# Kernel tuning notes

Measured on AMD Instinct MI355X. Metric: run time of the kernel, lower is better.

## Reference

```python
import jax, jax.numpy as jnp
import numpy as np

B, S, E, D = 2, 1024, 1024, 2048
H, KV, HD = 8, 4, 256
SOFTCAP = 50.0
SCALE = 256.0 ** -0.5  # query_pre_attn_scalar ** -0.5
WINDOW = 512
EPS = 1e-6
THETA = 10000.0


def setup_inputs() -> dict:
    key = jax.random.key(0)
    ks = jax.random.split(key, 10)
    hidden_states = jax.random.normal(ks[0], (B, S, D), jnp.float32)
    encoder_hidden_states = jax.random.normal(ks[1], (B, E, D), jnp.float32)
    # two packed segments per sequence (position resets at S//2)
    position_ids = jnp.broadcast_to(
        jnp.concatenate([jnp.arange(S // 2), jnp.arange(S - S // 2)]), (B, S)
    ).astype(jnp.int32)
    decoder_attention_mask = jnp.ones((B, S), jnp.int32)
    encoder_attention_mask = jnp.broadcast_to(
        (jnp.arange(E) < (E - 64)).astype(jnp.int32), (B, E))
    # RoPE tables from position ids
    inv_freq = 1.0 / (THETA ** (jnp.arange(0, HD, 2, dtype=jnp.float32) / HD))
    freqs = position_ids.astype(jnp.float32)[..., None] * inv_freq  # [B,S,HD/2]
    emb = jnp.concatenate([freqs, freqs], axis=-1)  # [B,S,HD]
    cos, sin = jnp.cos(emb), jnp.sin(emb)
    wq = 0.02 * jax.random.normal(ks[2], (D, H * HD), jnp.float32)
    wk = 0.02 * jax.random.normal(ks[3], (D, KV * HD), jnp.float32)
    wv = 0.02 * jax.random.normal(ks[4], (D, KV * HD), jnp.float32)
    wo = 0.02 * jax.random.normal(ks[5], (H * HD, D), jnp.float32)
    q_norm_w = 0.1 * jax.random.normal(ks[6], (HD,), jnp.float32)
    k_norm_w = 0.1 * jax.random.normal(ks[7], (HD,), jnp.float32)
    return dict(hidden_states=hidden_states,
                encoder_hidden_states=encoder_hidden_states,
                cos=cos, sin=sin, wq=wq, wk=wk, wv=wv, wo=wo,
                q_norm_w=q_norm_w, k_norm_w=k_norm_w,
                decoder_attention_mask=decoder_attention_mask,
                encoder_attention_mask=encoder_attention_mask,
                position_ids=position_ids)


def _rms_norm(x, w):
    # GemmaRMSNorm: x * rsqrt(mean(x^2)+eps) * (1 + w)
    var = jnp.mean(x * x, axis=-1, keepdims=True)
    return x * jax.lax.rsqrt(var + EPS) * (1.0 + w)


def _rotate_half(x):
    h = x.shape[-1] // 2
    return jnp.concatenate([-x[..., h:], x[..., :h]], axis=-1)


def _build_merged_mask(dec_mask, enc_mask, position_ids):
    dm = dec_mask.astype(bool)
    em = enc_mask.astype(bool)
    Sq = dm.shape[1]
    causal = jnp.tril(jnp.ones((Sq, Sq), bool))
    # segment ids from non-increasing position resets (packing)
    reset = jnp.concatenate(
        [jnp.ones((dm.shape[0], 1), bool),
         position_ids[:, 1:] <= position_ids[:, :-1]], axis=1)
    seg = jnp.cumsum(reset.astype(jnp.int32), axis=1)
    block = seg[:, :, None] == seg[:, None, :]
    full_self = dm[:, None, :] & causal[None] & block  # [B,S,S]
    rows = jnp.arange(Sq)
    dist = rows[:, None] - rows[None, :]
    sliding = (dist >= 0) & (dist < WINDOW)
    self_mask = full_self & sliding[None]
    cross = jnp.broadcast_to(em[:, None, :], (dm.shape[0], Sq, em.shape[1]))
    return jnp.concatenate([self_mask, cross], axis=-1)[:, None]  # [B,1,S,S+E]


def reference(hidden_states, encoder_hidden_states, cos, sin, wq, wk, wv, wo,
              q_norm_w, k_norm_w, decoder_attention_mask,
              encoder_attention_mask, position_ids):
    Bq, Sq, _ = hidden_states.shape
    Ek = encoder_hidden_states.shape[1]
    q = (hidden_states @ wq).reshape(Bq, Sq, H, HD).transpose(0, 2, 1, 3)
    k_self = (hidden_states @ wk).reshape(Bq, Sq, KV, HD).transpose(0, 2, 1, 3)
    v_self = (hidden_states @ wv).reshape(Bq, Sq, KV, HD).transpose(0, 2, 1, 3)
    k_cross = (encoder_hidden_states @ wk).reshape(Bq, Ek, KV, HD).transpose(0, 2, 1, 3)
    v_cross = (encoder_hidden_states @ wv).reshape(Bq, Ek, KV, HD).transpose(0, 2, 1, 3)
    # QK RMSNorm (cross keys normalized but NOT rotated, matching source)
    q = _rms_norm(q, q_norm_w)
    k_self = _rms_norm(k_self, k_norm_w)
    k_cross = _rms_norm(k_cross, k_norm_w)
    c, s = cos[:, None, :, :], sin[:, None, :, :]
    q = q * c + _rotate_half(q) * s
    k_self = k_self * c + _rotate_half(k_self) * s
    k = jnp.concatenate([k_self, k_cross], axis=2)  # [B,KV,S+E,HD]
    v = jnp.concatenate([v_self, v_cross], axis=2)
    rep = H // KV
    k = jnp.repeat(k, rep, axis=1)
    v = jnp.repeat(v, rep, axis=1)
    mask = _build_merged_mask(decoder_attention_mask, encoder_attention_mask,
                              position_ids)
    scores = jnp.einsum('bhqd,bhkd->bhqk', q, k) * SCALE
    scores = SOFTCAP * jnp.tanh(scores / SOFTCAP)  # logit softcapping
    scores = jnp.where(mask, scores, jnp.float32(-1e30))
    attn = jax.nn.softmax(scores, axis=-1)
    out = jnp.einsum('bhqk,bhkd->bhqd', attn, v)
    out = out.transpose(0, 2, 1, 3).reshape(Bq, Sq, H * HD)
    return out @ wo
```

## Files before the change

### kernel.cpp

```cpp
#include <hip/hip_runtime.h>
#include <math.h>

#define B_ 2
#define S_ 1024
#define E_ 1024
#define D_ 2048
#define H_ 8
#define KV_ 4
#define HD_ 256
#define WINDOW_ 512u
#define SCALE_ 0.0625f
#define CAP_ 50.0f
#define EPS_ 1e-6f
#define CROSS_OK (-7)
#define KINV (-2147483647 - 1)

typedef __bf16 bf8_t __attribute__((ext_vector_type(8)));
typedef float fx4 __attribute__((ext_vector_type(4)));
#define MFMA16(a, b, c) __builtin_amdgcn_mfma_f32_16x16x32_bf16((a), (b), (c), 0, 0, 0)

typedef __attribute__((address_space(1))) unsigned int gas_u32;
typedef __attribute__((address_space(3))) unsigned int las_u32;
__device__ __forceinline__ void gl2lds16(const void* g, void* l) {
    __builtin_amdgcn_global_load_lds((const gas_u32*)g, (las_u32*)l, 16, 0, 0);
}

union U4 { __bf16 b[4]; unsigned long long u; };

__device__ __forceinline__ float pexp(float dot) {
    float e = __expf(dot * (2.0f * SCALE_ / CAP_));
    return __expf(-(2.0f * CAP_) / (e + 1.0f));
}

__global__ __launch_bounds__(256) void tobf16(const float* __restrict__ x,
                                              __bf16* __restrict__ y, int n4) {
    int i = blockIdx.x * 256 + threadIdx.x;
    if (i >= n4) return;
    float4 v = ((const float4*)x)[i];
    U4 p;
    p.b[0] = (__bf16)v.x; p.b[1] = (__bf16)v.y;
    p.b[2] = (__bf16)v.z; p.b[3] = (__bf16)v.w;
    *(unsigned long long*)&y[(size_t)i * 4] = p.u;
}

__global__ __launch_bounds__(256) void tsplit(const float* __restrict__ W,
                                              __bf16* __restrict__ Th,
                                              __bf16* __restrict__ Tl, int K, int N) {
    __shared__ float tile[32][33];
    const int t = threadIdx.x, tx = t & 31, ty = t >> 5;
    const int k0 = blockIdx.x * 32, n0 = blockIdx.y * 32;
#pragma unroll
    for (int r = 0; r < 4; ++r)
        tile[ty + r * 8][tx] = W[(size_t)(k0 + ty + r * 8) * N + n0 + tx];
    __syncthreads();
#pragma unroll
    for (int r = 0; r < 4; ++r) {
        float v = tile[tx][ty + r * 8];
        __bf16 h = (__bf16)v;
        size_t o = (size_t)(n0 + ty + r * 8) * K + k0 + tx;
        Th[o] = h;
        Tl[o] = (__bf16)(v - (float)h);
    }
}

template <int NPASS>
__device__ __forceinline__ void gemm_core2(
    const __bf16* __restrict__ Ah, const __bf16* __restrict__ Al,
    const __bf16* __restrict__ Bh, const __bf16* __restrict__ Bl,
    int row0, int col0, int K,
    __bf16* As0, __bf16* As1, __bf16* Bs0, __bf16* Bs1, fx4 (&acc)[4][4]) {
    const int tid = threadIdx.x, lane = tid & 63, wv = tid >> 6;
    const int l15 = lane & 15, lq = lane >> 4;
    const int wm = (wv >> 1) * 64, wn = (wv & 1) * 64;
    constexpr int WCNT = (NPASS == 1) ? 0x0F74 : (NPASS == 2) ? 0x0F76 : 0x0F78;

    auto stage = [&](int buf, int k0) {
#pragma unroll
        for (int s = 0; s < 2; ++s) {
            int ch = (wv * 2 + s) * 64 + lane;
            int r = ch >> 2, cp = ch & 3;
            int cl = (cp - ((r >> 1) & 3)) & 3;
            size_t ga = (size_t)(row0 + r) * K + k0 + cl * 8;
            size_t gb = (size_t)(col0 + r) * K + k0 + cl * 8;
            gl2lds16(Ah + ga, As0 + buf * 4096 + ch * 8);
            if (NPASS >= 3) gl2lds16(Al + ga, As1 + buf * 4096 + ch * 8);
            gl2lds16(Bh + gb, Bs0 + buf * 4096 + ch * 8);
            if (NPASS >= 2) gl2lds16(Bl + gb, Bs1 + buf * 4096 + ch * 8);
        }
    };

    stage(0, 0);
    for (int k0 = 0; k0 < K; k0 += 32) {
        const int buf = (k0 >> 5) & 1;
        const bool hasnext = (k0 + 32 < K);
        if (hasnext) stage(buf ^ 1, k0 + 32);
        if (hasnext) __builtin_amdgcn_s_waitcnt(WCNT);
        else         __builtin_amdgcn_s_waitcnt(0x0F70);
        __builtin_amdgcn_s_barrier();
        __builtin_amdgcn_sched_barrier(0);

        const __bf16* A0 = As0 + buf * 4096;
        const __bf16* A1 = As1 + buf * 4096;
        const __bf16* B0 = Bs0 + buf * 4096;
        const __bf16* B1 = Bs1 + buf * 4096;
        bf8_t ah[4], al[4], bh[4], bl[4];
#pragma unroll
        for (int i = 0; i < 4; ++i) {
            int row = wm + i * 16 + l15;
            int sl = row * 4 + ((lq + (row >> 1)) & 3);
            ah[i] = *(const bf8_t*)(A0 + sl * 8);
            if (NPASS >= 3) al[i] = *(const bf8_t*)(A1 + sl * 8);
        }
#pragma unroll
        for (int j = 0; j < 4; ++j) {
            int row = wn + j * 16 + l15;
            int sl = row * 4 + ((lq + (row >> 1)) & 3);
            bh[j] = *(const bf8_t*)(B0 + sl * 8);
            if (NPASS >= 2) bl[j] = *(const bf8_t*)(B1 + sl * 8);
        }
#pragma unroll
        for (int i = 0; i < 4; ++i)
#pragma unroll
            for (int j = 0; j < 4; ++j) {
                acc[i][j] = MFMA16(ah[i], bh[j], acc[i][j]);
                if (NPASS >= 2) acc[i][j] = MFMA16(ah[i], bl[j], acc[i][j]);
                if (NPASS >= 3) acc[i][j] = MFMA16(al[i], bh[j], acc[i][j]);
            }
        __builtin_amdgcn_sched_barrier(0);
        __builtin_amdgcn_s_barrier();
    }
}

__global__ __launch_bounds__(256) void gemm_proj(
    const __bf16* __restrict__ hsb, const __bf16* __restrict__ encb,
    const __bf16* __restrict__ BTh, const __bf16* __restrict__ BTl,
    float* __restrict__ qf32, float* __restrict__ ksf, float* __restrict__ kcf,
    __bf16* __restrict__ vtS, __bf16* __restrict__ vtC) {
    __shared__ __bf16 As0[8192], Bs0[8192], Bs1[8192];
    const int bx = blockIdx.x, row0 = blockIdx.y * 128;
    const __bf16* A;
    float* Ck; __bf16* Cv; int col0;
    if (bx < 32) { A = hsb;  col0 = bx * 128;               Ck = ksf; Cv = vtS; }
    else         { A = encb; col0 = (bx - 32) * 128 + 2048; Ck = kcf; Cv = vtC; }
    fx4 acc[4][4];
#pragma unroll
    for (int i = 0; i < 4; ++i)
#pragma unroll
        for (int j = 0; j < 4; ++j) acc[i][j] = (fx4){0.f, 0.f, 0.f, 0.f};
    if (col0 >= 3072)
        gemm_core2<2>(A, nullptr, BTh, BTl, row0, col0, D_, As0, nullptr, Bs0, Bs1, acc);
    else
        gemm_core2<1>(A, nullptr, BTh, BTl, row0, col0, D_, As0, nullptr, Bs0, Bs1, acc);

    const int tid = threadIdx.x, lane = tid & 63, wv = tid >> 6;
    const int l15 = lane & 15, lq = lane >> 4;
    const int wm = (wv >> 1) * 64, wn = (wv & 1) * 64;
    const int mode = (col0 < 2048) ? 0 : (col0 < 3072 ? 1 : 2);
#pragma unroll
    for (int i = 0; i < 4; ++i)
#pragma unroll
        for (int j = 0; j < 4; ++j) {
            int mb = row0 + wm + i * 16 + lq * 4;
            int n = col0 + wn + j * 16 + l15;
            if (mode == 0) {
#pragma unroll
                for (int r = 0; r < 4; ++r)
                    qf32[(size_t)(mb + r) * 2048 + n] = acc[i][j][r];
            } else if (mode == 1) {
                int nk = n - 2048;
#pragma unroll
                for (int r = 0; r < 4; ++r)
                    Ck[(size_t)(mb + r) * 1024 + nk] = acc[i][j][r];
            } else {
                int nv = n - 3072;
                int b = mb >> 10, s = mb & 1023;
                int kv = nv >> 8, d = nv & 255;
                U4 pk;
#pragma unroll
                for (int r = 0; r < 4; ++r) pk.b[r] = (__bf16)acc[i][j][r];
                *(unsigned long long*)&Cv[((size_t)(b * KV_ + kv) * HD_ + d) * 1024 + s] = pk.u;
            }
        }
}

__global__ __launch_bounds__(256) void gemm_out(
    const __bf16* __restrict__ Ah, const __bf16* __restrict__ Al,
    const __bf16* __restrict__ Bh, const __bf16* __restrict__ Bl,
    float* __restrict__ C) {
    __shared__ __bf16 As0[8192], As1[8192], Bs0[8192], Bs1[8192];
    const int row0 = blockIdx.y * 128, col0 = blockIdx.x * 128;
    fx4 acc[4][4];
#pragma unroll
    for (int i = 0; i < 4; ++i)
#pragma unroll
        for (int j = 0; j < 4; ++j) acc[i][j] = (fx4){0.f, 0.f, 0.f, 0.f};
    gemm_core2<3>(Ah, Al, Bh, Bl, row0, col0, 2048, As0, As1, Bs0, Bs1, acc);
    const int tid = threadIdx.x, lane = tid & 63, wv = tid >> 6;
    const int l15 = lane & 15, lq = lane >> 4;
    const int wm = (wv >> 1) * 64, wn = (wv & 1) * 64;
#pragma unroll
    for (int i = 0; i < 4; ++i)
#pragma unroll
        for (int j = 0; j < 4; ++j) {
            int mb = row0 + wm + i * 16 + lq * 4;
            int n = col0 + wn + j * 16 + l15;
#pragma unroll
            for (int r = 0; r < 4; ++r)
                C[(size_t)(mb + r) * 2048 + n] = acc[i][j][r];
        }
}

__global__ __launch_bounds__(256) void rmsnorm_rope(const float* __restrict__ x,
                                                    __bf16* __restrict__ out,
                                                    const float* __restrict__ w,
                                                    const float* __restrict__ cs,
                                                    const float* __restrict__ sn,
                                                    int nheads, int do_rope, int trans) {
    const int tid = threadIdx.x;
    const size_t base = (size_t)blockIdx.x * HD_;
    float v = x[base + tid];
    float ss = v * v;
#pragma unroll
    for (int off = 32; off; off >>= 1) ss += __shfl_down(ss, off);
    __shared__ float red[4];
    __shared__ float ybuf[HD_];
    const int lane = tid & 63, wvi = tid >> 6;
    if (lane == 0) red[wvi] = ss;
    __syncthreads();
    float tot = red[0] + red[1] + red[2] + red[3];
    float scale = rsqrtf(tot * (1.0f / HD_) + EPS_);
    float y = v * scale * (1.0f + w[tid]);
    const int m = blockIdx.x / nheads;
    if (do_rope) {
        ybuf[tid] = y;
        __syncthreads();
        float rot = (tid < HD_ / 2) ? -ybuf[tid + HD_ / 2] : ybuf[tid - HD_ / 2];
        size_t coff = (size_t)m * HD_;
        y = y * cs[coff + tid] + rot * sn[coff + tid];
    }
    size_t oidx;
    if (trans) {
        int hh = blockIdx.x % nheads;
        int b = m >> 10, s = m & 1023;
        oidx = ((size_t)(b * nheads + hh) * 1024 + s) * HD_ + tid;
    } else {
        oidx = base + tid;
    }
    out[oidx] = (__bf16)y;
}

__global__ void segscan(const int* __restrict__ pos, const int* __restrict__ dm,
                        const int* __restrict__ em, int* __restrict__ seg,
                        int* __restrict__ ki) {
    const int b = blockIdx.x, s = threadIdx.x;
    __shared__ int sh[1024];
    int p = pos[b * S_ + s];
    int r = (s == 0) ? 1 : (p <= pos[b * S_ + s - 1] ? 1 : 0);
    sh[s] = r;
    __syncthreads();
    for (int off = 1; off < 1024; off <<= 1) {
        int v = sh[s];
        int u = (s >= off) ? sh[s - off] : 0;
        __syncthreads();
        sh[s] = v + u;
        __syncthreads();
    }
    int sv = sh[s];
    seg[b * S_ + s] = sv;
    ki[b * 2048 + s] = dm[b * S_ + s] ? sv : KINV;
    ki[b * 2048 + 1024 + s] = em[b * E_ + s] ? CROSS_OK : KINV;
}

__global__ __launch_bounds__(256, 1) void attn_part(
    const __bf16* __restrict__ qb,
    const __bf16* __restrict__ kb,
    const __bf16* __restrict__ kcb,
    const __bf16* __restrict__ vtS,
    const __bf16* __restrict__ vtC,
    const int* __restrict__ seg, const int* __restrict__ ki,
    float* __restrict__ accS, float* __restrict__ accC,
    float* __restrict__ lsS, float* __restrict__ lsC) {
    __shared__ __bf16 Ks[2][8192];
    __shared__ __bf16 Vs[2][8192];
    __shared__ __bf16 Ps[4][640];
    __shared__ int kinfoS[1024];
    const int tid = threadIdx.x, lane = tid & 63, wv = tid >> 6;
    const int l15 = lane & 15, lq = lane >> 4;
    const int bid = blockIdx.x;
    const int role = bid >> 8;
    const int g = bid & 7;
    const int b = g >> 2, kv = g & 3;
    const int rest = (bid >> 3) & 31;
    const int qt = rest >> 1, h = kv * 2 + (rest & 1);
    const int s0 = qt * 64;

    int lo = 0, nt = 32;
    const __bf16 *Kbase, *Vbase;
    if (role == 0) {
        lo = (s0 >= 512) ? ((s0 - 511) & ~31) : 0;
        nt = (s0 + 64 - lo) >> 5;
        Kbase = kb + (size_t)(b * KV_ + kv) * (1024 * 256);
        Vbase = vtS + (size_t)(b * KV_ + kv) * (256 * 1024);
    } else {
        Kbase = kcb + (size_t)(b * KV_ + kv) * (1024 * 256);
        Vbase = vtC + (size_t)(b * KV_ + kv) * (256 * 1024);
    }
    const int nk = nt * 32;
    const int kiofs = b * 2048 + (role ? 1024 : lo);
    for (int i = tid; i < nk; i += 256) kinfoS[i] = ki[kiofs + i];
    __syncthreads();

    const int qpos = s0 + wv * 16 + l15;
    bf8_t qf[8];
    const __bf16* qrow = qb + ((size_t)(b * S_ + qpos) * H_ + h) * HD_;
#pragma unroll
    for (int f = 0; f < 8; ++f) qf[f] = *(const bf8_t*)(qrow + f * 32 + lq * 8);
    const int tgt = role ? CROSS_OK : seg[b * S_ + qpos];

    auto stage = [&](int buf, int t) {
        const __bf16* Kt = Kbase + (size_t)(lo + t * 32) * 256;
        const __bf16* Vt = Vbase + (lo + t * 32);
#pragma unroll
        for (int r = 0; r < 4; ++r) {
            int cid = r * 256 + tid;
            int key = cid >> 5, c = cid & 31;
            gl2lds16(Kt + key * 256 + (((c ^ (key & 7))) << 3), &Ks[buf][cid * 8]);
        }
#pragma unroll
        for (int r = 0; r < 4; ++r) {
            int cid = r * 256 + tid;
            int d = cid >> 2, kc = cid & 3;
            gl2lds16(Vt + (size_t)d * 1024 + ((kc ^ ((d >> 1) & 3)) << 3),
                     &Vs[buf][cid * 8]);
        }
    };

    fx4 accO[16];
#pragma unroll
    for (int j = 0; j < 16; ++j) accO[j] = (fx4){0.f, 0.f, 0.f, 0.f};
    float lsum = 0.f;
    const int swzk = l15 & 7;
    const int swzv = lq ^ ((l15 >> 1) & 3);

    stage(0, 0);
    for (int i = 0; i < nt; ++i) {
        const int kt0_c = lo + i * 32;
        const int kio_c = i * 32;
        const bool hasnext = (i + 1 < nt);
        if (hasnext) stage((i + 1) & 1, i + 1);
        if (hasnext) __builtin_amdgcn_s_waitcnt(0x0F78);
        else         __builtin_amdgcn_s_waitcnt(0x0F70);
        __builtin_amdgcn_s_barrier();
        __builtin_amdgcn_sched_barrier(0);

        const __bf16* Ksb = Ks[i & 1];
        const __bf16* Vsb = Vs[i & 1];
        fx4 sc0 = (fx4){0.f, 0.f, 0.f, 0.f}, sc1 = (fx4){0.f, 0.f, 0.f, 0.f};
#pragma unroll
        for (int f = 0; f < 8; ++f) {
            bf8_t k0 = *(const bf8_t*)&Ksb[(l15 * 32 + ((f * 4 + lq) ^ swzk)) * 8];
            bf8_t k1 = *(const bf8_t*)&Ksb[((16 + l15) * 32 + ((f * 4 + lq) ^ swzk)) * 8];
            sc0 = MFMA16(k0, qf[f], sc0);
            sc1 = MFMA16(k1, qf[f], sc1);
        }
        int4 ki0 = *(const int4*)&kinfoS[kio_c + lq * 4];
        int4 ki1 = *(const int4*)&kinfoS[kio_c + 16 + lq * 4];
        int ka0[4] = {ki0.x, ki0.y, ki0.z, ki0.w};
        int ka1[4] = {ki1.x, ki1.y, ki1.z, ki1.w};
        U4 p0, p1;
#pragma unroll
        for (int r = 0; r < 4; ++r) {
            int key0 = kt0_c + lq * 4 + r;
            float e0 = pexp(sc0[r]);
            float e1 = pexp(sc1[r]);
            bool ok0 = (ka0[r] == tgt) && (role || (unsigned)(qpos - key0) < WINDOW_);
            bool ok1 = (ka1[r] == tgt) && (role || (unsigned)(qpos - key0 - 16) < WINDOW_);
            float v0 = ok0 ? e0 : 0.f;
            float v1 = ok1 ? e1 : 0.f;
            lsum += v0 + v1;
            p0.b[r] = (__bf16)v0;
            p1.b[r] = (__bf16)v1;
        }
        *(unsigned long long*)&Ps[wv][l15 * 40 + lq * 4] = p0.u;
        *(unsigned long long*)&Ps[wv][l15 * 40 + 16 + lq * 4] = p1.u;
        bf8_t pf = *(const bf8_t*)&Ps[wv][l15 * 40 + lq * 8];
#pragma unroll
        for (int j = 0; j < 16; ++j) {
            bf8_t vb = *(const bf8_t*)&Vsb[((j * 16 + l15) * 4 + swzv) * 8];
            accO[j] = MFMA16(pf, vb, accO[j]);
        }
        __builtin_amdgcn_sched_barrier(0);
        __builtin_amdgcn_s_barrier();
    }

    lsum += __shfl_xor(lsum, 16, 64);
    lsum += __shfl_xor(lsum, 32, 64);
    float* accT = role ? accC : accS;
    float* lsT  = role ? lsC  : lsS;
    if (lq == 0) lsT[(size_t)(b * S_ + qpos) * 8 + h] = lsum;
#pragma unroll
    for (int j = 0; j < 16; ++j)
#pragma unroll
        for (int r = 0; r < 4; ++r) {
            size_t idx = (size_t)(b * S_ + s0 + wv * 16 + lq * 4 + r) * 2048 +
                         h * 256 + j * 16 + l15;
            accT[idx] = accO[j][r];
        }
}

__global__ __launch_bounds__(256) void combine(
    const float* __restrict__ aS, const float* __restrict__ aC,
    const float* __restrict__ lS, const float* __restrict__ lC,
    __bf16* __restrict__ aH, __bf16* __restrict__ aL) {
    int i = blockIdx.x * 256 + threadIdx.x;
    size_t base = (size_t)i * 4;
    int row = (int)(base >> 11);
    int h = (int)((base >> 8) & 7);
    float inv = 1.0f / (lS[row * 8 + h] + lC[row * 8 + h]);
    float4 a = ((const float4*)aS)[i];
    float4 c = ((const float4*)aC)[i];
    float o[4] = {(a.x + c.x) * inv, (a.y + c.y) * inv,
                  (a.z + c.z) * inv, (a.w + c.w) * inv};
    U4 ph, pl;
#pragma unroll
    for (int r = 0; r < 4; ++r) {
        __bf16 hi = (__bf16)o[r];
        ph.b[r] = hi;
        pl.b[r] = (__bf16)(o[r] - (float)hi);
    }
    *(unsigned long long*)&aH[base] = ph.u;
    *(unsigned long long*)&aL[base] = pl.u;
}

extern "C" void kernel_launch(void* const* d_in, const int* in_sizes, int n_in,
                              void* d_out, int out_size, void* d_ws, size_t ws_size,
                              hipStream_t stream) {
    (void)in_sizes; (void)n_in; (void)out_size; (void)ws_size;
    const float* hs  = (const float*)d_in[0];
    const float* enc = (const float*)d_in[1];
    const float* cs  = (const float*)d_in[2];
    const float* sn  = (const float*)d_in[3];
    const float* wq  = (const float*)d_in[4];
    const float* wk  = (const float*)d_in[5];
    const float* wv  = (const float*)d_in[6];
    const float* wo  = (const float*)d_in[7];
    const float* qnw = (const float*)d_in[8];
    const float* knw = (const float*)d_in[9];
    const int* dm    = (const int*)d_in[10];
    const int* em    = (const int*)d_in[11];
    const int* pos   = (const int*)d_in[12];
    float* out = (float*)d_out;

    char* ws = (char*)d_ws;
    const size_t MB = 1ull << 20;
    __bf16* hs_bf   = (__bf16*)(ws + 0 * MB);
    __bf16* enc_bf  = (__bf16*)(ws + 8 * MB);
    __bf16* wqkvTH  = (__bf16*)(ws + 16 * MB);
    __bf16* wqkvTL  = (__bf16*)(ws + 32 * MB);
    __bf16* woTH    = (__bf16*)(ws + 48 * MB);
    __bf16* woTL    = (__bf16*)(ws + 56 * MB);
    float*  qf32    = (float*)(ws + 64 * MB);
    float*  ksf     = (float*)(ws + 80 * MB);
    float*  kcf     = (float*)(ws + 88 * MB);
    __bf16* k_bf    = (__bf16*)(ws + 104 * MB);
    __bf16* kc_bf   = (__bf16*)(ws + 108 * MB);
    __bf16* vtS     = (__bf16*)(ws + 112 * MB);
    __bf16* vtC     = (__bf16*)(ws + 116 * MB);
    int*    seg     = (int*)(ws + 120 * MB);
    int*    kinfo   = (int*)(ws + 121 * MB);
    __bf16* q_bf    = (__bf16*)(ws + 124 * MB);
    __bf16* aoutH   = (__bf16*)(ws + 0 * MB);
    __bf16* aoutL   = (__bf16*)(ws + 9 * MB);
    float*  accS    = (float*)(ws + 64 * MB);
    float*  accC    = (float*)(ws + 81 * MB);
    float*  lsS     = (float*)(ws + 98 * MB);
    float*  lsC     = (float*)(ws + 99 * MB);

    const int M = B_ * S_;

    tobf16<<<4096, 256, 0, stream>>>(hs, hs_bf, M * D_ / 4);
    tobf16<<<4096, 256, 0, stream>>>(enc, enc_bf, M * D_ / 4);
    tsplit<<<dim3(64, 64), 256, 0, stream>>>(wq, wqkvTH, wqkvTL, D_, 2048);
    tsplit<<<dim3(64, 32), 256, 0, stream>>>(wk, wqkvTH + (size_t)2048 * 2048,
                                             wqkvTL + (size_t)2048 * 2048, D_, 1024);
    tsplit<<<dim3(64, 32), 256, 0, stream>>>(wv, wqkvTH + (size_t)3072 * 2048,
                                             wqkvTL + (size_t)3072 * 2048, D_, 1024);
    tsplit<<<dim3(64, 64), 256, 0, stream>>>(wo, woTH, woTL, 2048, D_);

    gemm_proj<<<dim3(48, 16), 256, 0, stream>>>(hs_bf, enc_bf, wqkvTH, wqkvTL,
                                                qf32, ksf, kcf, vtS, vtC);

    rmsnorm_rope<<<16384, 256, 0, stream>>>(qf32, q_bf, qnw, cs, sn, H_, 1, 0);
    rmsnorm_rope<<<8192, 256, 0, stream>>>(ksf, k_bf, knw, cs, sn, KV_, 1, 1);
    rmsnorm_rope<<<8192, 256, 0, stream>>>(kcf, kc_bf, knw, cs, sn, KV_, 0, 1);
    segscan<<<B_, 1024, 0, stream>>>(pos, dm, em, seg, kinfo);

    attn_part<<<512, 256, 0, stream>>>(q_bf, k_bf, kc_bf, vtS, vtC, seg, kinfo,
                                       accS, accC, lsS, lsC);
    combine<<<4096, 256, 0, stream>>>(accS, accC, lsS, lsC, aoutH, aoutL);

    gemm_out<<<dim3(16, 16), 256, 0, stream>>>(aoutH, aoutL, woTH, woTL, out);
}
```

Measured before the change: 428.6 us.

## Merge prep launches, skip unused weight low halves, enlarge projection GEMM tiles

Folds the two bf16 conversions, four weight transpose-splits and the segment scan into a single prep kernel. The low-half bf16 writes for wq and wk are dropped, since the projection GEMM only does the high pass for those columns. The segment scan is rewritten with wave shuffles instead of a 1024-thread shared-memory scan. The QKV projection GEMM moves to 512-thread blocks covering 256 rows, reusing each B tile across more rows, and the three RMSNorm/RoPE launches become one. The aim is to cut launch overhead and memory traffic, at the cost of more branching in the merged kernels and fewer, larger GEMM blocks.

```diff
diff --git a/kernel.cpp b/kernel.cpp
--- a/kernel.cpp
+++ b/kernel.cpp
@@ -32,9 +32,8 @@
     return __expf(-(2.0f * CAP_) / (e + 1.0f));
 }
 
-__global__ __launch_bounds__(256) void tobf16(const float* __restrict__ x,
-                                              __bf16* __restrict__ y, int n4) {
-    int i = blockIdx.x * 256 + threadIdx.x;
+__device__ __forceinline__ void dev_tobf16(const float* __restrict__ x,
+                                           __bf16* __restrict__ y, int n4, int i) {
     if (i >= n4) return;
     float4 v = ((const float4*)x)[i];
     U4 p;
@@ -43,12 +42,13 @@
     *(unsigned long long*)&y[(size_t)i * 4] = p.u;
 }
 
-__global__ __launch_bounds__(256) void tsplit(const float* __restrict__ W,
-                                              __bf16* __restrict__ Th,
-                                              __bf16* __restrict__ Tl, int K, int N) {
-    __shared__ float tile[32][33];
-    const int t = threadIdx.x, tx = t & 31, ty = t >> 5;
-    const int k0 = blockIdx.x * 32, n0 = blockIdx.y * 32;
+__device__ __forceinline__ void dev_tsplit(const float* __restrict__ W,
+                                           __bf16* __restrict__ Th,
+                                           __bf16* __restrict__ Tl, int K, int N,
+                                           int bx, int by, int t,
+                                           float (*tile)[33], int wlo) {
+    const int tx = t & 31, ty = t >> 5;
+    const int k0 = bx * 32, n0 = by * 32;
 #pragma unroll
     for (int r = 0; r < 4; ++r)
         tile[ty + r * 8][tx] = W[(size_t)(k0 + ty + r * 8) * N + n0 + tx];
@@ -59,8 +59,89 @@
         __bf16 h = (__bf16)v;
         size_t o = (size_t)(n0 + ty + r * 8) * K + k0 + tx;
         Th[o] = h;
-        Tl[o] = (__bf16)(v - (float)h);
-    }
+        if (wlo) Tl[o] = (__bf16)(v - (float)h);
+    }
+}
+
+__device__ __forceinline__ void dev_segscan(const int* __restrict__ pos,
+                                            const int* __restrict__ dm,
+                                            const int* __restrict__ em,
+                                            int* __restrict__ seg,
+                                            int* __restrict__ ki,
+                                            int b, int t, int* wsum) {
+    const int base = b * 1024 + t * 4;
+    int4 p = *(const int4*)&pos[base];
+    int pm1 = (t == 0) ? 0 : pos[base - 1];
+    int r0 = (t == 0) ? 1 : (p.x <= pm1 ? 1 : 0);
+    int r1 = (p.y <= p.x), r2 = (p.z <= p.y), r3 = (p.w <= p.z);
+    int c0 = r0, c1 = c0 + r1, c2 = c1 + r2, c3 = c2 + r3;
+    const int lane = t & 63, wv = t >> 6;
+    int x = c3;
+#pragma unroll
+    for (int off = 1; off < 64; off <<= 1) {
+        int y = __shfl_up(x, off, 64);
+        if (lane >= off) x += y;
+    }
+    if (lane == 63) wsum[wv] = x;
+    __syncthreads();
+    int woff = 0;
+#pragma unroll
+    for (int w = 0; w < 4; ++w) if (w < wv) woff += wsum[w];
+    const int excl = woff + x - c3;
+    int sv[4] = {excl + c0, excl + c1, excl + c2, excl + c3};
+    int4 dmv = *(const int4*)&dm[base];
+    int4 emv = *(const int4*)&em[base];
+    int dma[4] = {dmv.x, dmv.y, dmv.z, dmv.w};
+    int ema[4] = {emv.x, emv.y, emv.z, emv.w};
+#pragma unroll
+    for (int r = 0; r < 4; ++r) {
+        seg[base + r] = sv[r];
+        ki[b * 2048 + t * 4 + r] = dma[r] ? sv[r] : KINV;
+        ki[b * 2048 + 1024 + t * 4 + r] = ema[r] ? CROSS_OK : KINV;
+    }
+}
+
+__global__ __launch_bounds__(256) void prep(
+    const float* __restrict__ hs, const float* __restrict__ enc,
+    const float* __restrict__ wq, const float* __restrict__ wk,
+    const float* __restrict__ wvp, const float* __restrict__ wo,
+    const int* __restrict__ pos, const int* __restrict__ dm,
+    const int* __restrict__ em,
+    __bf16* __restrict__ hs_bf, __bf16* __restrict__ enc_bf,
+    __bf16* __restrict__ wqkvTH, __bf16* __restrict__ wqkvTL,
+    __bf16* __restrict__ woTH, __bf16* __restrict__ woTL,
+    int* __restrict__ seg, int* __restrict__ ki) {
+    __shared__ float tile[32][33];
+    __shared__ int wsum[4];
+    int bid = blockIdx.x;
+    const int t = threadIdx.x;
+    if (bid < 4096) { dev_tobf16(hs, hs_bf, 1048576, bid * 256 + t); return; }
+    bid -= 4096;
+    if (bid < 4096) { dev_tobf16(enc, enc_bf, 1048576, bid * 256 + t); return; }
+    bid -= 4096;
+    if (bid < 4096) {
+        dev_tsplit(wq, wqkvTH, nullptr, 2048, 2048, bid & 63, bid >> 6, t, tile, 0);
+        return;
+    }
+    bid -= 4096;
+    if (bid < 2048) {
+        dev_tsplit(wk, wqkvTH + (size_t)2048 * 2048, nullptr, 2048, 1024,
+                   bid & 63, bid >> 6, t, tile, 0);
+        return;
+    }
+    bid -= 2048;
+    if (bid < 2048) {
+        dev_tsplit(wvp, wqkvTH + (size_t)3072 * 2048, wqkvTL + (size_t)3072 * 2048,
+                   2048, 1024, bid & 63, bid >> 6, t, tile, 1);
+        return;
+    }
+    bid -= 2048;
+    if (bid < 4096) {
+        dev_tsplit(wo, woTH, woTL, 2048, 2048, bid & 63, bid >> 6, t, tile, 1);
+        return;
+    }
+    bid -= 4096;
+    dev_segscan(pos, dm, em, seg, ki, bid, t, wsum);
 }
 
 template <int NPASS>
@@ -131,13 +212,82 @@
     }
 }
 
-__global__ __launch_bounds__(256) void gemm_proj(
+template <int NPASS>
+__device__ __forceinline__ void gemm_core3(
+    const __bf16* __restrict__ Ah,
+    const __bf16* __restrict__ Bh, const __bf16* __restrict__ Bl,
+    int row0, int col0, int K,
+    __bf16* As0, __bf16* Bs0, __bf16* Bs1, fx4 (&acc)[4][4]) {
+    const int tid = threadIdx.x, lane = tid & 63, wv = tid >> 6;
+    const int l15 = lane & 15, lq = lane >> 4;
+    const int wm = (wv >> 1) * 64, wn = (wv & 1) * 64;
+    constexpr int WCNT = (NPASS == 1) ? 0x0F73 : 0x0F74;
+
+    auto stage = [&](int buf, int k0) {
+#pragma unroll
+        for (int s = 0; s < 2; ++s) {
+            int ch = s * 512 + tid;
+            int r = ch >> 2, cp = ch & 3;
+            int cl = (cp - ((r >> 1) & 3)) & 3;
+            size_t ga = (size_t)(row0 + r) * K + k0 + cl * 8;
+            gl2lds16(Ah + ga, As0 + buf * 8192 + ch * 8);
+        }
+        {
+            int ch = tid;
+            int r = ch >> 2, cp = ch & 3;
+            int cl = (cp - ((r >> 1) & 3)) & 3;
+            size_t gb = (size_t)(col0 + r) * K + k0 + cl * 8;
+            gl2lds16(Bh + gb, Bs0 + buf * 4096 + ch * 8);
+            if (NPASS >= 2) gl2lds16(Bl + gb, Bs1 + buf * 4096 + ch * 8);
+        }
+    };
+
+    stage(0, 0);
+    for (int k0 = 0; k0 < K; k0 += 32) {
+        const int buf = (k0 >> 5) & 1;
+        const bool hasnext = (k0 + 32 < K);
+        if (hasnext) stage(buf ^ 1, k0 + 32);
+        if (hasnext) __builtin_amdgcn_s_waitcnt(WCNT);
+        else         __builtin_amdgcn_s_waitcnt(0x0F70);
+        __builtin_amdgcn_s_barrier();
+        __builtin_amdgcn_sched_barrier(0);
+
+        const __bf16* A0 = As0 + buf * 8192;
+        const __bf16* B0 = Bs0 + buf * 4096;
+        const __bf16* B1 = Bs1 + buf * 4096;
+        bf8_t ah[4], bh[4], bl[4];
+#pragma unroll
+        for (int i = 0; i < 4; ++i) {
+            int row = wm + i * 16 + l15;
+            int sl = row * 4 + ((lq + (row >> 1)) & 3);
+            ah[i] = *(const bf8_t*)(A0 + sl * 8);
+        }
+#pragma unroll
+        for (int j = 0; j < 4; ++j) {
+            int row = wn + j * 16 + l15;
+            int sl = row * 4 + ((lq + (row >> 1)) & 3);
+            bh[j] = *(const bf8_t*)(B0 + sl * 8);
+            if (NPASS >= 2) bl[j] = *(const bf8_t*)(B1 + sl * 8);
+        }
+#pragma unroll
+        for (int i = 0; i < 4; ++i)
+#pragma unroll
+            for (int j = 0; j < 4; ++j) {
+                acc[i][j] = MFMA16(ah[i], bh[j], acc[i][j]);
+                if (NPASS >= 2) acc[i][j] = MFMA16(ah[i], bl[j], acc[i][j]);
+            }
+        __builtin_amdgcn_sched_barrier(0);
+        __builtin_amdgcn_s_barrier();
+    }
+}
+
+__global__ __launch_bounds__(512) void gemm_proj(
     const __bf16* __restrict__ hsb, const __bf16* __restrict__ encb,
     const __bf16* __restrict__ BTh, const __bf16* __restrict__ BTl,
     float* __restrict__ qf32, float* __restrict__ ksf, float* __restrict__ kcf,
     __bf16* __restrict__ vtS, __bf16* __restrict__ vtC) {
-    __shared__ __bf16 As0[8192], Bs0[8192], Bs1[8192];
-    const int bx = blockIdx.x, row0 = blockIdx.y * 128;
+    __shared__ __bf16 As0[16384], Bs0[8192], Bs1[8192];
+    const int bx = blockIdx.x, row0 = blockIdx.y * 256;
     const __bf16* A;
     float* Ck; __bf16* Cv; int col0;
     if (bx < 32) { A = hsb;  col0 = bx * 128;               Ck = ksf; Cv = vtS; }
@@ -148,9 +298,9 @@
 #pragma unroll
         for (int j = 0; j < 4; ++j) acc[i][j] = (fx4){0.f, 0.f, 0.f, 0.f};
     if (col0 >= 3072)
-        gemm_core2<2>(A, nullptr, BTh, BTl, row0, col0, D_, As0, nullptr, Bs0, Bs1, acc);
+        gemm_core3<2>(A, BTh, BTl, row0, col0, D_, As0, Bs0, Bs1, acc);
     else
-        gemm_core2<1>(A, nullptr, BTh, BTl, row0, col0, D_, As0, nullptr, Bs0, Bs1, acc);
+        gemm_core3<1>(A, BTh, BTl, row0, col0, D_, As0, Bs0, Bs1, acc);
 
     const int tid = threadIdx.x, lane = tid & 63, wv = tid >> 6;
     const int l15 = lane & 15, lq = lane >> 4;
@@ -210,14 +360,21 @@
         }
 }
 
-__global__ __launch_bounds__(256) void rmsnorm_rope(const float* __restrict__ x,
-                                                    __bf16* __restrict__ out,
-                                                    const float* __restrict__ w,
-                                                    const float* __restrict__ cs,
-                                                    const float* __restrict__ sn,
-                                                    int nheads, int do_rope, int trans) {
+__global__ __launch_bounds__(256) void rms_all(
+    const float* __restrict__ qf32, const float* __restrict__ ksf,
+    const float* __restrict__ kcf,
+    __bf16* __restrict__ q_bf, __bf16* __restrict__ k_bf,
+    __bf16* __restrict__ kc_bf,
+    const float* __restrict__ qnw, const float* __restrict__ knw,
+    const float* __restrict__ cs, const float* __restrict__ sn) {
+    int bid = blockIdx.x;
+    const float* x; __bf16* out; const float* w;
+    int nheads, do_rope, trans;
+    if (bid < 16384)      { x = qf32; out = q_bf;  w = qnw; nheads = 8; do_rope = 1; trans = 0; }
+    else if (bid < 24576) { bid -= 16384; x = ksf; out = k_bf;  w = knw; nheads = 4; do_rope = 1; trans = 1; }
+    else                  { bid -= 24576; x = kcf; out = kc_bf; w = knw; nheads = 4; do_rope = 0; trans = 1; }
     const int tid = threadIdx.x;
-    const size_t base = (size_t)blockIdx.x * HD_;
+    const size_t base = (size_t)bid * HD_;
     float v = x[base + tid];
     float ss = v * v;
 #pragma unroll
@@ -230,7 +387,7 @@
     float tot = red[0] + red[1] + red[2] + red[3];
     float scale = rsqrtf(tot * (1.0f / HD_) + EPS_);
     float y = v * scale * (1.0f + w[tid]);
-    const int m = blockIdx.x / nheads;
+    const int m = bid / nheads;
     if (do_rope) {
         ybuf[tid] = y;
         __syncthreads();
@@ -240,35 +397,13 @@
     }
     size_t oidx;
     if (trans) {
-        int hh = blockIdx.x % nheads;
+        int hh = bid % nheads;
         int b = m >> 10, s = m & 1023;
         oidx = ((size_t)(b * nheads + hh) * 1024 + s) * HD_ + tid;
     } else {
         oidx = base + tid;
     }
     out[oidx] = (__bf16)y;
-}
-
-__global__ void segscan(const int* __restrict__ pos, const int* __restrict__ dm,
-                        const int* __restrict__ em, int* __restrict__ seg,
-                        int* __restrict__ ki) {
-    const int b = blockIdx.x, s = threadIdx.x;
-    __shared__ int sh[1024];
-    int p = pos[b * S_ + s];
-    int r = (s == 0) ? 1 : (p <= pos[b * S_ + s - 1] ? 1 : 0);
-    sh[s] = r;
-    __syncthreads();
-    for (int off = 1; off < 1024; off <<= 1) {
-        int v = sh[s];
-        int u = (s >= off) ? sh[s - off] : 0;
-        __syncthreads();
-        sh[s] = v + u;
-        __syncthreads();
-    }
-    int sv = sh[s];
-    seg[b * S_ + s] = sv;
-    ki[b * 2048 + s] = dm[b * S_ + s] ? sv : KINV;
-    ki[b * 2048 + 1024 + s] = em[b * E_ + s] ? CROSS_OK : KINV;
 }
 
 __global__ __launch_bounds__(256, 1) void attn_part(
@@ -476,24 +611,15 @@
     float*  lsS     = (float*)(ws + 98 * MB);
     float*  lsC     = (float*)(ws + 99 * MB);
 
-    const int M = B_ * S_;
-
-    tobf16<<<4096, 256, 0, stream>>>(hs, hs_bf, M * D_ / 4);
-    tobf16<<<4096, 256, 0, stream>>>(enc, enc_bf, M * D_ / 4);
-    tsplit<<<dim3(64, 64), 256, 0, stream>>>(wq, wqkvTH, wqkvTL, D_, 2048);
-    tsplit<<<dim3(64, 32), 256, 0, stream>>>(wk, wqkvTH + (size_t)2048 * 2048,
-                                             wqkvTL + (size_t)2048 * 2048, D_, 1024);
-    tsplit<<<dim3(64, 32), 256, 0, stream>>>(wv, wqkvTH + (size_t)3072 * 2048,
-                                             wqkvTL + (size_t)3072 * 2048, D_, 1024);
-    tsplit<<<dim3(64, 64), 256, 0, stream>>>(wo, woTH, woTL, 2048, D_);
-
-    gemm_proj<<<dim3(48, 16), 256, 0, stream>>>(hs_bf, enc_bf, wqkvTH, wqkvTL,
-                                                qf32, ksf, kcf, vtS, vtC);
-
-    rmsnorm_rope<<<16384, 256, 0, stream>>>(qf32, q_bf, qnw, cs, sn, H_, 1, 0);
-    rmsnorm_rope<<<8192, 256, 0, stream>>>(ksf, k_bf, knw, cs, sn, KV_, 1, 1);
-    rmsnorm_rope<<<8192, 256, 0, stream>>>(kcf, kc_bf, knw, cs, sn, KV_, 0, 1);
-    segscan<<<B_, 1024, 0, stream>>>(pos, dm, em, seg, kinfo);
+    prep<<<20482, 256, 0, stream>>>(hs, enc, wq, wk, wv, wo, pos, dm, em,
+                                    hs_bf, enc_bf, wqkvTH, wqkvTL, woTH, woTL,
+                                    seg, kinfo);
+
+    gemm_proj<<<dim3(48, 8), 512, 0, stream>>>(hs_bf, enc_bf, wqkvTH, wqkvTL,
+                                               qf32, ksf, kcf, vtS, vtC);
+
+    rms_all<<<32768, 256, 0, stream>>>(qf32, ksf, kcf, q_bf, k_bf, kc_bf,
+                                       qnw, knw, cs, sn);
 
     attn_part<<<512, 256, 0, stream>>>(q_bf, k_bf, kc_bf, vtS, vtC, seg, kinfo,
                                        accS, accC, lsS, lsC);
```

After: 419.4 us. -2.1%, faster.
